# Optimization experiments

Measured on AMD Instinct MI355X. Metric: run time of the kernel, lower is better.

## Reference

```python
import jax, jax.numpy as jnp
import numpy as np

EMBED, HEADS, LEVELS, POINTS, MLP = 256, 8, 3, 4, 4
SHAPES = [(60, 80), (30, 40), (15, 20)]  # (H, W) per level


def layer_norm(x, g, b):
    m = jnp.mean(x, -1, keepdims=True)
    v = jnp.mean((x - m) ** 2, -1, keepdims=True)
    return (x - m) * jax.lax.rsqrt(v + 1e-5) * g + b


def _bilinear(v, H, W, gx, gy):
    # v: [B,h,H*W,dh]; gx,gy: [B,h,Nq,P] absolute pixel coords (grid_sample align_corners=False, zero padding)
    x0 = jnp.floor(gx); y0 = jnp.floor(gy)
    wx = gx - x0; wy = gy - y0

    def g(xi, yi):
        valid = ((xi >= 0) & (xi < W) & (yi >= 0) & (yi < H)).astype(v.dtype)
        idx = jnp.clip(yi, 0, H - 1) * W + jnp.clip(xi, 0, W - 1)
        B, h, Nq, P = idx.shape
        out = jnp.take_along_axis(v, idx.reshape(B, h, Nq * P)[..., None], axis=2)
        return out.reshape(B, h, Nq, P, -1) * valid[..., None]

    x0i = x0.astype(jnp.int32); y0i = y0.astype(jnp.int32)
    return (g(x0i, y0i) * ((1 - wx) * (1 - wy))[..., None]
            + g(x0i + 1, y0i) * (wx * (1 - wy))[..., None]
            + g(x0i, y0i + 1) * ((1 - wx) * wy)[..., None]
            + g(x0i + 1, y0i + 1) * (wx * wy)[..., None])


def setup_inputs() -> dict:
    key = jax.random.key(0)
    ks = jax.random.split(key, 16)
    B, Nq, C = 2, 8192, EMBED
    Nv = sum(h * w for h, w in SHAPES)
    s = 0.02
    d = {
        'query': jax.random.normal(ks[0], (B, Nq, C), jnp.float32),
        'value': jax.random.normal(ks[1], (B, Nv, C), jnp.float32),
        'query_pos': jax.random.normal(ks[2], (B, Nq, C), jnp.float32),
        'ref_pts': jax.random.uniform(ks[3], (B, Nq, LEVELS, 2), jnp.float32),
        'spatial_shapes': jnp.array(SHAPES, jnp.int32),
        'level_start_index': jnp.array(np.cumsum([0] + [h * w for h, w in SHAPES[:-1]]), jnp.int32),
        'g1': jnp.ones((C,), jnp.float32), 'b1': jnp.zeros((C,), jnp.float32),
        'Wo': s * jax.random.normal(ks[4], (C, HEADS * LEVELS * POINTS * 2), jnp.float32),
        'bo': jnp.zeros((HEADS * LEVELS * POINTS * 2,), jnp.float32),
        'Wa': s * jax.random.normal(ks[5], (C, HEADS * LEVELS * POINTS), jnp.float32),
        'ba': jnp.zeros((HEADS * LEVELS * POINTS,), jnp.float32),
        'Wv': s * jax.random.normal(ks[6], (C, C), jnp.float32), 'bv': jnp.zeros((C,), jnp.float32),
        'Wp': s * jax.random.normal(ks[7], (C, C), jnp.float32), 'bp': jnp.zeros((C,), jnp.float32),
        'g2': jnp.ones((C,), jnp.float32), 'b2': jnp.zeros((C,), jnp.float32),
        'Wf1': s * jax.random.normal(ks[8], (C, MLP * C), jnp.float32), 'bf1': jnp.zeros((MLP * C,), jnp.float32),
        'Wf2': s * jax.random.normal(ks[9], (MLP * C, C), jnp.float32), 'bf2': jnp.zeros((C,), jnp.float32),
    }
    return d


def reference(query, value, query_pos, ref_pts, spatial_shapes, level_start_index,
              g1, b1, Wo, bo, Wa, ba, Wv, bv, Wp, bp, g2, b2, Wf1, bf1, Wf2, bf2):
    B, Nq, C = query.shape
    dh = C // HEADS
    shapes = np.asarray(spatial_shapes).tolist()
    starts = np.asarray(level_start_index).tolist()

    qn = layer_norm(query, g1, b1)           # pre-norm
    qa = qn + query_pos                       # positional embedding inside attn
    offs = (qa @ Wo + bo).reshape(B, Nq, HEADS, LEVELS, POINTS, 2)
    aw = jax.nn.softmax((qa @ Wa + ba).reshape(B, Nq, HEADS, LEVELS * POINTS), -1)
    aw = aw.reshape(B, Nq, HEADS, LEVELS, POINTS)
    v = (value @ Wv + bv).reshape(B, -1, HEADS, dh).transpose(0, 2, 1, 3)  # [B,h,Nv,dh]

    # offset_normalizer = (W, H) per level
    norm = jnp.array([[w, h] for h, w in shapes], jnp.float32)
    loc = ref_pts[:, :, None, :, None, :] + offs / norm[None, None, None, :, None, :]

    out = jnp.zeros((B, Nq, HEADS, dh), query.dtype)
    for l, (H, W) in enumerate(shapes):
        vl = jax.lax.dynamic_slice_in_dim(v, starts[l], H * W, axis=2)
        gl = loc[:, :, :, l].transpose(0, 2, 1, 3, 4)   # [B,h,Nq,P,2]
        gx = gl[..., 0] * W - 0.5
        gy = gl[..., 1] * H - 0.5
        sampled = _bilinear(vl, H, W, gx, gy)            # [B,h,Nq,P,dh]
        out = out + jnp.einsum('bhqpd,bqhp->bqhd', sampled, aw[:, :, :, l])

    attn = out.reshape(B, Nq, C) @ Wp + bp + qn          # output proj + mmcv internal residual (identity=norm1(query))
    q = query + attn                                     # layer residual
    q2 = layer_norm(q, g2, b2)
    return q + (jax.nn.gelu(q2 @ Wf1 + bf1, approximate=False) @ Wf2 + bf2)
```

## Files before the change

kernel.cpp:

```cpp
#include <hip/hip_runtime.h>
#include <math.h>


typedef short short8 __attribute__((ext_vector_type(8)));
typedef short s16x4 __attribute__((ext_vector_type(4)));
typedef __bf16 bf16x8 __attribute__((ext_vector_type(8)));
typedef float f32x4 __attribute__((ext_vector_type(4)));

__device__ __forceinline__ short f2b(float f) {
  unsigned u = __builtin_bit_cast(unsigned, f);
  u += 0x7fffu + ((u >> 16) & 1u);
  return (short)(u >> 16);
}
__device__ __forceinline__ float b2f(short s) {
  unsigned u = ((unsigned)(unsigned short)s) << 16;
  return __builtin_bit_cast(float, u);
}
__device__ __forceinline__ void b8f(short8 s, float* f) {
  const uint4 u = __builtin_bit_cast(uint4, s);
  f[0] = __builtin_bit_cast(float, u.x << 16);
  f[1] = __builtin_bit_cast(float, u.x & 0xffff0000u);
  f[2] = __builtin_bit_cast(float, u.y << 16);
  f[3] = __builtin_bit_cast(float, u.y & 0xffff0000u);
  f[4] = __builtin_bit_cast(float, u.z << 16);
  f[5] = __builtin_bit_cast(float, u.z & 0xffff0000u);
  f[6] = __builtin_bit_cast(float, u.w << 16);
  f[7] = __builtin_bit_cast(float, u.w & 0xffff0000u);
}

__device__ __forceinline__ f32x4 mfma16(short8 a, short8 b, f32x4 c) {
  return __builtin_amdgcn_mfma_f32_16x16x32_bf16(
      __builtin_bit_cast(bf16x8, a), __builtin_bit_cast(bf16x8, b), c, 0, 0, 0);
}

typedef __attribute__((address_space(3))) unsigned int lds_u32;
typedef const __attribute__((address_space(1))) unsigned int glb_u32;
__device__ __forceinline__ void glds16(const void* g, void* l) {
  __builtin_amdgcn_global_load_lds((glb_u32*)g, (lds_u32*)l, 16, 0, 0);
}

__device__ __forceinline__ float gelu1(float v) {
  return 0.5f * v * (1.f + erff(v * 0.70710678118654752f));
}

template <int EPI>
__device__ __forceinline__ void gemm64_core(
    int bx, int by,
    const short* __restrict__ A, const short* __restrict__ Bt,
    const float* __restrict__ bias, const float* __restrict__ bias2,
    void* __restrict__ Cout, int M, int Nreal, int ldc, int K, char* smem)
{
  short* sA = (short*)smem;
  short* sB = sA + 4096;
  float* sf = (float*)smem;

  const int t = threadIdx.x;
  const int wave = t >> 6, lane = t & 63;
  const int quad = lane >> 4, l16 = lane & 15;
  const int wm = (wave & 1) * 32, wn = (wave >> 1) * 64;
  const int m0 = by * 64, n0 = bx * 128;

  f32x4 acc[2][4];
#pragma unroll
  for (int i = 0; i < 2; i++)
#pragma unroll
    for (int j = 0; j < 4; j++) acc[i][j] = (f32x4){0.f, 0.f, 0.f, 0.f};

  const int srow = lane >> 3, pos = lane & 7;
  const int chunk = (pos + srow) & 7;
  const short* gA = A + (size_t)(m0 + wave * 16 + srow) * K + chunk * 8;
  const short* gB = Bt + (size_t)(n0 + wave * 32 + srow) * K + chunk * 8;

  const int nk = K >> 6;
  for (int kt = 0; kt < nk; ++kt) {
    if (kt) __syncthreads();
    const int ko = kt * 64;
#pragma unroll
    for (int g = 0; g < 2; ++g)
      glds16(gA + ko + (size_t)(g * 8) * K, sA + (wave * 16 + g * 8) * 64);
#pragma unroll
    for (int g = 0; g < 4; ++g)
      glds16(gB + ko + (size_t)(g * 8) * K, sB + (wave * 32 + g * 8) * 64);
    __syncthreads();
#pragma unroll
    for (int kk = 0; kk < 2; ++kk) {
      short8 af[2], bf[4];
      const int c = kk * 4 + quad;
#pragma unroll
      for (int i = 0; i < 2; i++) {
        const int lrA = wm + i * 16 + l16;
        af[i] = *(const short8*)&sA[lrA * 64 + ((c - lrA) & 7) * 8];
      }
#pragma unroll
      for (int j = 0; j < 4; j++) {
        const int lrB = wn + j * 16 + l16;
        bf[j] = *(const short8*)&sB[lrB * 64 + ((c - lrB) & 7) * 8];
      }
#pragma unroll
      for (int i = 0; i < 2; i++)
#pragma unroll
        for (int j = 0; j < 4; j++) acc[i][j] = mfma16(bf[j], af[i], acc[i][j]);
    }
  }
  __syncthreads();

#pragma unroll
  for (int b = 0; b < 2; ++b) {
    if (wm == b * 32) {
#pragma unroll
      for (int i = 0; i < 2; ++i) {
        const int rr = i * 16 + l16;
#pragma unroll
        for (int j = 0; j < 4; ++j)
          *(f32x4*)&sf[rr * 132 + wn + quad * 4 + j * 16] = acc[i][j];
      }
    }
    __syncthreads();
#pragma unroll
    for (int r2 = 0; r2 < 4; ++r2) {
      const int fidx = r2 * 1024 + t * 4;
      const int row = fidx >> 7, col = fidx & 127;
      const int gm = m0 + b * 32 + row;
      const int cc = n0 + col;
      if (gm < M && cc < Nreal) {
        const float4 v = *(const float4*)&sf[row * 132 + col];
        float4 bb;
        if (EPI == 4) bb = (cc < 192) ? *(const float4*)(bias + cc)
                                      : *(const float4*)(bias2 + cc - 192);
        else bb = *(const float4*)(bias + cc);
        float v0 = v.x + bb.x, v1 = v.y + bb.y, v2 = v.z + bb.z, v3 = v.w + bb.w;
        s16x4 o; o.x = f2b(v0); o.y = f2b(v1); o.z = f2b(v2); o.w = f2b(v3);
        *(s16x4*)((short*)Cout + (size_t)gm * ldc + cc) = o;
      }
    }
    __syncthreads();
  }
}

__global__ __launch_bounds__(256) void gemm_oa_v(
    const short* __restrict__ qa, const short* __restrict__ wt_oa,
    const float* __restrict__ bo, const float* __restrict__ ba,
    short* __restrict__ oabuf,
    const short* __restrict__ valbf, const short* __restrict__ wt_v,
    const float* __restrict__ bv, short* __restrict__ vproj)
{
  __shared__ __align__(16) char smem[24576];
  const int idx = blockIdx.x;
  if (idx < 768) {
    gemm64_core<4>(idx % 3, idx / 3, qa, wt_oa, bo, ba,
                   oabuf, 16384, 288, 288, 256, smem);
  } else {
    const int r = idx - 768;
    gemm64_core<5>(r % 2, r / 2, valbf, wt_v, bv, nullptr,
                   vproj, 12600, 256, 256, 256, smem);
  }
}

__global__ __launch_bounds__(1024, 4) void wp_mlp(
    const short* __restrict__ sampled,
    const short* __restrict__ wtp,
    const float* __restrict__ bp,
    const short* __restrict__ qnb,
    const float* __restrict__ query,
    const float* __restrict__ g2, const float* __restrict__ b2v,
    const short* __restrict__ wf1,
    const float* __restrict__ b1v,
    const short* __restrict__ wf2,
    const float* __restrict__ bf2v,
    float* __restrict__ outp)
{
  __shared__ __align__(16) char smem[99328];
  float* sf = (float*)smem;
  short* H  = (short*)smem;
  short* RA = (short*)(smem + 66560);

  const int t = threadIdx.x;
  const int w = t >> 6, lane = t & 63;
  const int quad = lane >> 4, l16 = lane & 15;
  const int wm2 = w >> 3, wn8 = w & 7;
  const int m0 = blockIdx.x * 64;

#pragma unroll
  for (int q = 0; q < 2; ++q) {
    const int row = q * 32 + w * 2 + (lane >> 5);
    const int pos = lane & 31;
    const int cl = (pos & ~7) | ((pos + row) & 7);
    glds16(sampled + (size_t)(m0 + row) * 256 + cl * 8, RA + q * 8192 + w * 512);
  }
  __syncthreads();

  {
    f32x4 accp[2][2];
#pragma unroll
    for (int i = 0; i < 2; i++)
#pragma unroll
      for (int j = 0; j < 2; j++) accp[i][j] = (f32x4){0.f, 0.f, 0.f, 0.f};
#pragma unroll
    for (int kk = 0; kk < 8; ++kk) {
      const int c = kk * 4 + quad;
      short8 bfr[2], afr[2];
#pragma unroll
      for (int j = 0; j < 2; ++j) {
        const int n1 = wn8 * 2 + j;
        bfr[j] = *(const short8*)(wtp + ((size_t)n1 * 32 + c) * 128 + l16 * 8);
      }
#pragma unroll
      for (int i = 0; i < 2; ++i) {
        const int r = wm2 * 32 + i * 16 + l16;
        const int pos = (c & ~7) | ((c - r) & 7);
        afr[i] = *(const short8*)(RA + r * 256 + pos * 8);
      }
#pragma unroll
      for (int i = 0; i < 2; ++i)
#pragma unroll
        for (int j = 0; j < 2; ++j) accp[i][j] = mfma16(bfr[j], afr[i], accp[i][j]);
    }
#pragma unroll
    for (int i = 0; i < 2; ++i)
#pragma unroll
      for (int j = 0; j < 2; ++j)
        *(f32x4*)&sf[(wm2 * 32 + i * 16 + l16) * 260 + wn8 * 32 + j * 16 + quad * 4] =
            accp[i][j];
  }
  __syncthreads();

  float4 qb[4];
  {
    const float4 bbp  = *(const float4*)(bp + lane * 4);
    const float4 gv   = *(const float4*)(g2 + lane * 4);
    const float4 bb2  = *(const float4*)(b2v + lane * 4);
#pragma unroll
    for (int rep = 0; rep < 4; ++rep) {
      const int row = rep * 16 + w;
      const int gm = m0 + row;
      const float4 a = *(const float4*)&sf[row * 260 + lane * 4];
      const s16x4 qn = *(const s16x4*)(qnb + (size_t)gm * 256 + lane * 4);
      const float4 qv = *(const float4*)(query + (size_t)gm * 256 + lane * 4);
      float v0 = a.x + bbp.x + b2f(qn.x) + qv.x;
      float v1 = a.y + bbp.y + b2f(qn.y) + qv.y;
      float v2 = a.z + bbp.z + b2f(qn.z) + qv.z;
      float v3 = a.w + bbp.w + b2f(qn.w) + qv.w;
      float s = v0 + v1 + v2 + v3;
#pragma unroll
      for (int o = 32; o; o >>= 1) s += __shfl_xor(s, o);
      const float mean = s * (1.f / 256.f);
      const float d0 = v0 - mean, d1 = v1 - mean, d2 = v2 - mean, d3 = v3 - mean;
      float ss = d0 * d0 + d1 * d1 + d2 * d2 + d3 * d3;
#pragma unroll
      for (int o = 32; o; o >>= 1) ss += __shfl_xor(ss, o);
      const float inv = rsqrtf(ss * (1.f / 256.f) + 1e-5f);
      qb[rep] = make_float4(v0, v1, v2, v3);
      const int col = lane * 4;
      const int c = col >> 3;
      const int pos = (c & ~7) | ((c - row) & 7);
      s16x4 o2;
      o2.x = f2b(d0 * inv * gv.x + bb2.x);
      o2.y = f2b(d1 * inv * gv.y + bb2.y);
      o2.z = f2b(d2 * inv * gv.z + bb2.z);
      o2.w = f2b(d3 * inv * gv.w + bb2.w);
      *(s16x4*)(RA + row * 256 + pos * 8 + (col & 7)) = o2;
    }
  }
  __syncthreads();

  f32x4 acc2[2][2];
#pragma unroll
  for (int i = 0; i < 2; i++)
#pragma unroll
    for (int j = 0; j < 2; j++) acc2[i][j] = (f32x4){0.f, 0.f, 0.f, 0.f};

  for (int h = 0; h < 2; ++h) {
    if (h) __syncthreads();
    f32x4 acc[4][2];
#pragma unroll
    for (int i = 0; i < 4; i++)
#pragma unroll
      for (int j = 0; j < 2; j++) acc[i][j] = (f32x4){0.f, 0.f, 0.f, 0.f};
#pragma unroll
    for (int kk = 0; kk < 8; ++kk) {
      const int cg = kk * 4 + quad;
      short8 bfr[2], afr[4];
#pragma unroll
      for (int j = 0; j < 2; ++j) {
        const int n1 = h * 32 + w * 2 + j;
        bfr[j] = *(const short8*)(wf1 + ((size_t)n1 * 32 + cg) * 128 + l16 * 8);
      }
#pragma unroll
      for (int i = 0; i < 4; ++i) {
        const int r = i * 16 + l16;
        const int pos = (cg & ~7) | ((cg - r) & 7);
        afr[i] = *(const short8*)(RA + r * 256 + pos * 8);
      }
#pragma unroll
      for (int i = 0; i < 4; ++i)
#pragma unroll
        for (int j = 0; j < 2; ++j) acc[i][j] = mfma16(bfr[j], afr[i], acc[i][j]);
    }
#pragma unroll
    for (int j = 0; j < 2; ++j) {
      const int coll = (w * 2 + j) * 16 + quad * 4;
      const float4 bb = *(const float4*)(b1v + h * 512 + coll);
      const int c = coll >> 3;
#pragma unroll
      for (int i = 0; i < 4; ++i) {
        const int r = i * 16 + l16;
        const int pos = (c & ~7) | ((c - r) & 7);
        s16x4 o;
        o.x = f2b(gelu1(acc[i][j].x + bb.x));
        o.y = f2b(gelu1(acc[i][j].y + bb.y));
        o.z = f2b(gelu1(acc[i][j].z + bb.z));
        o.w = f2b(gelu1(acc[i][j].w + bb.w));
        *(s16x4*)(H + r * 512 + pos * 8 + (coll & 7)) = o;
      }
    }
    __syncthreads();

#pragma unroll 4
    for (int kk = 0; kk < 16; ++kk) {
      const int cl = kk * 4 + quad;
      short8 bfr[2], afr[2];
#pragma unroll
      for (int j = 0; j < 2; ++j) {
        const int n1 = wn8 * 2 + j;
        bfr[j] = *(const short8*)(wf2 + ((size_t)n1 * 128 + h * 64 + cl) * 128 + l16 * 8);
      }
#pragma unroll
      for (int i = 0; i < 2; ++i) {
        const int r = wm2 * 32 + i * 16 + l16;
        const int pos = (cl & ~7) | ((cl - r) & 7);
        afr[i] = *(const short8*)(H + r * 512 + pos * 8);
      }
#pragma unroll
      for (int i = 0; i < 2; ++i)
#pragma unroll
        for (int j = 0; j < 2; ++j) acc2[i][j] = mfma16(bfr[j], afr[i], acc2[i][j]);
    }
  }
  __syncthreads();

#pragma unroll
  for (int i = 0; i < 2; ++i)
#pragma unroll
    for (int j = 0; j < 2; ++j)
      *(f32x4*)&sf[(wm2 * 32 + i * 16 + l16) * 260 + wn8 * 32 + j * 16 + quad * 4] =
          acc2[i][j];
  __syncthreads();

  {
    const float4 bbf = *(const float4*)(bf2v + lane * 4);
#pragma unroll
    for (int rep = 0; rep < 4; ++rep) {
      const int row = rep * 16 + w;
      const int gm = m0 + row;
      const float4 v = *(const float4*)&sf[row * 260 + lane * 4];
      *(float4*)(outp + (size_t)gm * 256 + lane * 4) =
          make_float4(v.x + bbf.x + qb[rep].x, v.y + bbf.y + qb[rep].y,
                      v.z + bbf.z + qb[rep].z, v.w + bbf.w + qb[rep].w);
    }
  }
}

__global__ __launch_bounds__(256) void prep_all(
    const float* __restrict__ Wo, const float* __restrict__ Wa,
    const float* __restrict__ Wv, const float* __restrict__ Wp,
    const float* __restrict__ Wf1, const float* __restrict__ Wf2,
    short* __restrict__ t_oa, short* __restrict__ t_v, short* __restrict__ t_p,
    short* __restrict__ t_f1, short* __restrict__ t_f2,
    const float* __restrict__ value, short* __restrict__ valbf,
    const float* __restrict__ query, const float* __restrict__ query_pos,
    const float* __restrict__ g1, const float* __restrict__ b1,
    short* __restrict__ qnb, short* __restrict__ qa)
{
  __shared__ float tile[32][33];
  const int t = threadIdx.x;
  const int blk = blockIdx.x;

  if (blk < 1792) {
    const int bxa = blk & 255, bya = blk >> 8;
    int K, N, noff; const float* src; short* dst;
    switch (bya) {
      case 0: src = Wo;      dst = t_oa; K = 256;  N = 192;  noff = 0;   break;
      case 1: src = Wa;      dst = t_oa; K = 256;  N = 96;   noff = 192; break;
      case 2: src = nullptr; dst = t_oa; K = 256;  N = 96;   noff = 288; break;
      case 3: src = Wv;      dst = t_v;  K = 256;  N = 256;  noff = 0;   break;
      case 4: src = Wp;      dst = t_p;  K = 256;  N = 256;  noff = 0;   break;
      case 5: src = Wf1;     dst = t_f1; K = 256;  N = 1024; noff = 0;   break;
      default: src = Wf2;    dst = t_f2; K = 1024; N = 256;  noff = 0;   break;
    }
    const bool fragpack = (bya >= 4);
    const int tilesK = K >> 5;
    const int nt = tilesK * (N >> 5);
    if (bxa >= nt) return;
    const int tk = bxa % tilesK, tn = bxa / tilesK;
    const int k0 = tk * 32, n0 = tn * 32;
    const int r = t >> 3, c4 = (t & 7) * 4;
    float4 v = make_float4(0.f, 0.f, 0.f, 0.f);
    if (src) v = *(const float4*)(src + (size_t)(k0 + r) * N + n0 + c4);
    tile[r][c4] = v.x; tile[r][c4 + 1] = v.y; tile[r][c4 + 2] = v.z; tile[r][c4 + 3] = v.w;
    __syncthreads();
    const int nn = t >> 3, kc = (t & 7) * 4;
    s16x4 o;
    o.x = f2b(tile[kc][nn]); o.y = f2b(tile[kc + 1][nn]);
    o.z = f2b(tile[kc + 2][nn]); o.w = f2b(tile[kc + 3][nn]);
    if (fragpack) {
      const int n = n0 + nn, k = k0 + kc;
      *(s16x4*)(dst + ((size_t)(n >> 4) * (K >> 3) + (k >> 3)) * 128 +
                (n & 15) * 8 + (k & 7)) = o;
    } else {
      *(s16x4*)(dst + (size_t)(noff + n0 + nn) * K + k0 + kc) = o;
    }
  } else if (blk < 1792 + 3169) {
    const int i = ((blk - 1792) * 256 + t) * 4;
    if (i >= 12672 * 256) return;
    s16x4 o = (s16x4){0, 0, 0, 0};
    if (i < 12600 * 256) {
      float4 v = *(const float4*)(value + i);
      o.x = f2b(v.x); o.y = f2b(v.y); o.z = f2b(v.z); o.w = f2b(v.w);
    }
    *(s16x4*)(valbf + i) = o;
  } else {
    const int row  = (blk - 4961) * 4 + (t >> 6);
    const int lane = t & 63;
    const float4 v = ((const float4*)(query + (size_t)row * 256))[lane];
    float s = v.x + v.y + v.z + v.w;
#pragma unroll
    for (int o = 32; o; o >>= 1) s += __shfl_xor(s, o);
    const float mean = s * (1.f / 256.f);
    const float dx = v.x - mean, dy = v.y - mean, dz = v.z - mean, dw = v.w - mean;
    float s2 = dx * dx + dy * dy + dz * dz + dw * dw;
#pragma unroll
    for (int o = 32; o; o >>= 1) s2 += __shfl_xor(s2, o);
    const float inv = rsqrtf(s2 * (1.f / 256.f) + 1e-5f);
    const float4 gv = ((const float4*)g1)[lane];
    const float4 bv = ((const float4*)b1)[lane];
    const float4 o1 = make_float4(dx * inv * gv.x + bv.x, dy * inv * gv.y + bv.y,
                                  dz * inv * gv.z + bv.z, dw * inv * gv.w + bv.w);
    s16x4 ob; ob.x = f2b(o1.x); ob.y = f2b(o1.y); ob.z = f2b(o1.z); ob.w = f2b(o1.w);
    ((s16x4*)(qnb + (size_t)row * 256))[lane] = ob;
    const float4 pv = ((const float4*)(query_pos + (size_t)row * 256))[lane];
    s16x4 op;
    op.x = f2b(o1.x + pv.x); op.y = f2b(o1.y + pv.y);
    op.z = f2b(o1.z + pv.z); op.w = f2b(o1.w + pv.w);
    ((s16x4*)(qa + (size_t)row * 256))[lane] = op;
  }
}

__global__ __launch_bounds__(256) void deform_fused(
    const short* __restrict__ vproj, const short* __restrict__ oa,
    const float* __restrict__ refp, short* __restrict__ out)
{
  __shared__ int4 sIdx[768];
  __shared__ s16x4 sW[768];
  const int t = threadIdx.x;

  if (t < 64) {
    const int row = blockIdx.x * 8 + (t >> 3), h = t & 7;
    const short* oarow = oa + (size_t)row * 288;
    float off[24];
    {
      const short8* op = (const short8*)(oarow + h * 24);
      b8f(op[0], off); b8f(op[1], off + 8); b8f(op[2], off + 16);
    }
    float lg[12];
    {
      const s16x4* ap = (const s16x4*)(oarow + 192 + h * 12);
#pragma unroll
      for (int i = 0; i < 3; i++) {
        const s16x4 v = ap[i];
        lg[i * 4] = b2f(v.x); lg[i * 4 + 1] = b2f(v.y);
        lg[i * 4 + 2] = b2f(v.z); lg[i * 4 + 3] = b2f(v.w);
      }
    }
    const float* rp = refp + (size_t)row * 6;
    const float Rx[3] = {rp[0], rp[2], rp[4]}, Ry[3] = {rp[1], rp[3], rp[5]};
    float mx = lg[0];
#pragma unroll
    for (int i = 1; i < 12; i++) mx = fmaxf(mx, lg[i]);
    float sum = 0.f;
#pragma unroll
    for (int i = 0; i < 12; i++) { lg[i] = __expf(lg[i] - mx); sum += lg[i]; }
    const float inv = 1.f / sum;
    const int b = row >> 13;
    const int Hs[3] = {60, 30, 15}, Ws[3] = {80, 40, 20}, St[3] = {0, 4800, 6000};
#pragma unroll
    for (int p = 0; p < 12; p++) {
      const int l = p >> 2;
      const int W = Ws[l], H = Hs[l];
      const float gx = Rx[l] * W + off[p * 2]     - 0.5f;
      const float gy = Ry[l] * H + off[p * 2 + 1] - 0.5f;
      const float x0f = floorf(gx), y0f = floorf(gy);
      const float wx = gx - x0f, wy = gy - y0f;
      const int x0 = (int)x0f, y0 = (int)y0f;
      const float aw = lg[p] * inv;
      float cw[4] = {(1.f - wx) * (1.f - wy), wx * (1.f - wy),
                     (1.f - wx) * wy, wx * wy};
      const int base = b * 6300 + St[l];
      int ci[4];
#pragma unroll
      for (int k = 0; k < 4; k++) {
        const int xx = x0 + (k & 1), yy = y0 + (k >> 1);
        const bool valid = (xx >= 0) & (xx < W) & (yy >= 0) & (yy < H);
        const int xc = min(max(xx, 0), W - 1);
        const int yc = min(max(yy, 0), H - 1);
        ci[k] = ((base + yc * W + xc) << 8) + h * 32;
        cw[k] = valid ? cw[k] * aw : 0.f;
      }
      sIdx[t * 12 + p] = make_int4(ci[0], ci[1], ci[2], ci[3]);
      s16x4 wv; wv.x = f2b(cw[0]); wv.y = f2b(cw[1]); wv.z = f2b(cw[2]); wv.w = f2b(cw[3]);
      sW[t * 12 + p] = wv;
    }
  }
  __syncthreads();

  const int lu = t >> 2, c4 = (t & 3) * 8;
  float acc[8];
#pragma unroll
  for (int i = 0; i < 8; i++) acc[i] = 0.f;
#pragma unroll 2
  for (int p = 0; p < 12; p++) {
    const int4 idx = sIdx[lu * 12 + p];
    const s16x4 wb = sW[lu * 12 + p];
    const float w0 = b2f(wb.x), w1 = b2f(wb.y), w2 = b2f(wb.z), w3 = b2f(wb.w);
    const short8 v0 = *(const short8*)(vproj + idx.x + c4);
    const short8 v1 = *(const short8*)(vproj + idx.y + c4);
    const short8 v2 = *(const short8*)(vproj + idx.z + c4);
    const short8 v3 = *(const short8*)(vproj + idx.w + c4);
    float f0[8], f1[8], f2[8], f3[8];
    b8f(v0, f0); b8f(v1, f1); b8f(v2, f2); b8f(v3, f3);
#pragma unroll
    for (int j = 0; j < 8; j++)
      acc[j] += w0 * f0[j] + w1 * f1[j] + w2 * f2[j] + w3 * f3[j];
  }
  short8 o;
#pragma unroll
  for (int j = 0; j < 8; j++) o[j] = f2b(acc[j]);
  *(short8*)(out + (size_t)(blockIdx.x * 256 + t) * 8) = o;
}

extern "C" void kernel_launch(void* const* d_in, const int* in_sizes, int n_in,
                              void* d_out, int out_size, void* d_ws, size_t ws_size,
                              hipStream_t stream)
{
  const float* query     = (const float*)d_in[0];
  const float* value     = (const float*)d_in[1];
  const float* query_pos = (const float*)d_in[2];
  const float* ref_pts   = (const float*)d_in[3];
  const float* g1  = (const float*)d_in[6];
  const float* b1  = (const float*)d_in[7];
  const float* Wo  = (const float*)d_in[8];
  const float* bo  = (const float*)d_in[9];
  const float* Wa  = (const float*)d_in[10];
  const float* ba  = (const float*)d_in[11];
  const float* Wv  = (const float*)d_in[12];
  const float* bv  = (const float*)d_in[13];
  const float* Wp  = (const float*)d_in[14];
  const float* bp  = (const float*)d_in[15];
  const float* g2  = (const float*)d_in[16];
  const float* b2  = (const float*)d_in[17];
  const float* Wf1 = (const float*)d_in[18];
  const float* bf1 = (const float*)d_in[19];
  const float* Wf2 = (const float*)d_in[20];
  const float* bf2 = (const float*)d_in[21];

  char* ws = (char*)d_ws;
  short* wt_oa   = (short*)(ws + 0);
  short* wt_v    = (short*)(ws + 196608);
  short* wt_p    = (short*)(ws + 327680);
  short* wt_f1   = (short*)(ws + 458752);
  short* wt_f2   = (short*)(ws + 983040);
  short* qnb     = (short*)(ws + 1507328);
  short* qa      = (short*)(ws + 18284544);
  short* oabuf   = (short*)(ws + 26673152);
  short* vproj   = (short*)(ws + 45547520);
  short* sampled = (short*)(ws + 51998720);
  short* valbf   = (short*)(ws + 77164544);
  float* outp = (float*)d_out;

  prep_all<<<9057, 256, 0, stream>>>(Wo, Wa, Wv, Wp, Wf1, Wf2,
                                     wt_oa, wt_v, wt_p, wt_f1, wt_f2,
                                     value, valbf, query, query_pos,
                                     g1, b1, qnb, qa);
  gemm_oa_v<<<1162, 256, 0, stream>>>(qa, wt_oa, bo, ba, oabuf,
                                      valbf, wt_v, bv, vproj);
  deform_fused<<<2048, 256, 0, stream>>>(vproj, oabuf, ref_pts, sampled);
  wp_mlp<<<256, 1024, 0, stream>>>(sampled, wt_p, bp, qnb, query, g2, b2,
                                   wt_f1, bf1, wt_f2, bf2, outp);
}
```

Before: 207.5 us.

## Prefetch query into LDS, keep residual in LDS, swizzle fp32 staging

In the wp_mlp kernel, the query rows are now loaded asynchronously from global memory into LDS at the same time as the sampled tile, rather than read from global memory in the LayerNorm stage. The residual that was held in registers (qb) is written back into LDS and reread in the epilogue. The padded fp32 staging rows (stride 260) are replaced by 256-wide rows with an XOR swizzle to avoid bank conflicts. Shared memory grows to 160 KB, the whole LDS of a CU, which leaves no headroom but should not change occupancy, since the 1024-thread block already ran one block per CU.

```diff
diff --git a/kernel.cpp b/kernel.cpp
--- a/kernel.cpp
+++ b/kernel.cpp
@@ -169,10 +169,11 @@
     const float* __restrict__ bf2v,
     float* __restrict__ outp)
 {
-  __shared__ __align__(16) char smem[99328];
-  float* sf = (float*)smem;
-  short* H  = (short*)smem;
-  short* RA = (short*)(smem + 66560);
+  __shared__ __align__(16) char smem[163840];
+  float* Q  = (float*)smem;
+  short* H  = (short*)(smem + 65536);
+  float* QY = (float*)(smem + 65536);
+  short* RA = (short*)(smem + 131072);
 
   const int t = threadIdx.x;
   const int w = t >> 6, lane = t & 63;
@@ -187,6 +188,11 @@
     const int cl = (pos & ~7) | ((pos + row) & 7);
     glds16(sampled + (size_t)(m0 + row) * 256 + cl * 8, RA + q * 8192 + w * 512);
   }
+#pragma unroll
+  for (int q = 0; q < 4; ++q) {
+    const int row = q * 16 + w;
+    glds16(query + (size_t)(m0 + row) * 256 + lane * 4, QY + row * 256);
+  }
   __syncthreads();
 
   {
@@ -218,13 +224,14 @@
 #pragma unroll
     for (int i = 0; i < 2; ++i)
 #pragma unroll
-      for (int j = 0; j < 2; ++j)
-        *(f32x4*)&sf[(wm2 * 32 + i * 16 + l16) * 260 + wn8 * 32 + j * 16 + quad * 4] =
-            accp[i][j];
+      for (int j = 0; j < 2; ++j) {
+        const int r = wm2 * 32 + i * 16 + l16;
+        const int c = wn8 * 32 + j * 16 + quad * 4;
+        *(f32x4*)&Q[r * 256 + (c ^ ((r & 7) << 2))] = accp[i][j];
+      }
   }
   __syncthreads();
 
-  float4 qb[4];
   {
     const float4 bbp  = *(const float4*)(bp + lane * 4);
     const float4 gv   = *(const float4*)(g2 + lane * 4);
@@ -233,9 +240,10 @@
     for (int rep = 0; rep < 4; ++rep) {
       const int row = rep * 16 + w;
       const int gm = m0 + row;
-      const float4 a = *(const float4*)&sf[row * 260 + lane * 4];
-      const s16x4 qn = *(const s16x4*)(qnb + (size_t)gm * 256 + lane * 4);
-      const float4 qv = *(const float4*)(query + (size_t)gm * 256 + lane * 4);
+      const int cs = (lane * 4) ^ ((row & 7) << 2);
+      const float4 a  = *(const float4*)&Q[row * 256 + cs];
+      const float4 qv = *(const float4*)&QY[row * 256 + lane * 4];
+      const s16x4 qn  = *(const s16x4*)(qnb + (size_t)gm * 256 + lane * 4);
       float v0 = a.x + bbp.x + b2f(qn.x) + qv.x;
       float v1 = a.y + bbp.y + b2f(qn.y) + qv.y;
       float v2 = a.z + bbp.z + b2f(qn.z) + qv.z;
@@ -249,7 +257,7 @@
 #pragma unroll
       for (int o = 32; o; o >>= 1) ss += __shfl_xor(ss, o);
       const float inv = rsqrtf(ss * (1.f / 256.f) + 1e-5f);
-      qb[rep] = make_float4(v0, v1, v2, v3);
+      *(f32x4*)&Q[row * 256 + cs] = (f32x4){v0, v1, v2, v3};
       const int col = lane * 4;
       const int c = col >> 3;
       const int pos = (c & ~7) | ((c - row) & 7);
@@ -341,9 +349,11 @@
 #pragma unroll
   for (int i = 0; i < 2; ++i)
 #pragma unroll
-    for (int j = 0; j < 2; ++j)
-      *(f32x4*)&sf[(wm2 * 32 + i * 16 + l16) * 260 + wn8 * 32 + j * 16 + quad * 4] =
-          acc2[i][j];
+    for (int j = 0; j < 2; ++j) {
+      const int r = wm2 * 32 + i * 16 + l16;
+      const int c = wn8 * 32 + j * 16 + quad * 4;
+      *(f32x4*)&QY[r * 256 + (c ^ ((r & 7) << 2))] = acc2[i][j];
+    }
   __syncthreads();
 
   {
@@ -352,10 +362,12 @@
     for (int rep = 0; rep < 4; ++rep) {
       const int row = rep * 16 + w;
       const int gm = m0 + row;
-      const float4 v = *(const float4*)&sf[row * 260 + lane * 4];
+      const int cs = (lane * 4) ^ ((row & 7) << 2);
+      const float4 v  = *(const float4*)&QY[row * 256 + cs];
+      const float4 qb = *(const float4*)&Q[row * 256 + cs];
       *(float4*)(outp + (size_t)gm * 256 + lane * 4) =
-          make_float4(v.x + bbf.x + qb[rep].x, v.y + bbf.y + qb[rep].y,
-                      v.z + bbf.z + qb[rep].z, v.w + bbf.w + qb[rep].w);
+          make_float4(v.x + bbf.x + qb.x, v.y + bbf.y + qb.y,
+                      v.z + bbf.z + qb.z, v.w + bbf.w + qb.w);
     }
   }
 }
```

Result: slower. 214.8 us (+3.5%).
